# Kernel optimization log

Measured on AMD Instinct MI355X. Metric: run time of the kernel, lower is better.

Reference implementation:

```python
import jax, jax.numpy as jnp
import numpy as np

H1, W1 = 16, 16  # SparseAttBlock stride
EPS = 1e-5       # BatchNorm eps


def _att(x, wx, bx, wy, by, wo, bo, gamma, beta):
    """DotProductAttBlock: 1x1 q/k projections, full softmax attention over
    the H*W tokens of each (small) block, then 1x1 conv + BatchNorm(train) + ReLU."""
    B, C, H, W = x.shape
    xf = x.reshape(B, C, H * W)                                  # [B,C,N]
    theta = jnp.einsum('mc,bcn->bnm', wx, xf) + bx               # [B,N,fmid]
    psi = jnp.einsum('mc,bcn->bmn', wy, xf) + by[:, None]        # [B,fmid,N]
    alpha = jax.nn.softmax(jnp.einsum('bnm,bmk->bnk', theta, psi), axis=2)  # [B,N,N]
    agg = jnp.einsum('bnk,bck->bcn', alpha, xf)                  # [B,C,N]
    out = jnp.einsum('oc,bcn->bon', wo, agg) + bo[:, None]       # [B,fout,N]
    # BatchNorm2d in training mode: biased batch stats over (batch, spatial)
    mean = out.mean(axis=(0, 2), keepdims=True)
    var = ((out - mean) ** 2).mean(axis=(0, 2), keepdims=True)
    out = (out - mean) * jax.lax.rsqrt(var + EPS) * gamma[:, None] + beta[:, None]
    return jax.nn.relu(out).reshape(B, -1, H, W)


def _forward(x, p1, p2):
    B, C, H, W = x.shape
    h2, w2 = H // H1, W // W1
    # pass 1: attention within each (H1,W1) block, blocks folded into batch
    xb = x.reshape(B, C, H1, h2, W1, w2).transpose(0, 3, 5, 1, 2, 4)
    xb = xb.reshape(B * h2 * w2, C, H1, W1)
    xb = _att(xb, *p1)
    # pass 2: attention across the (h2,w2) block grid
    xb = xb.reshape(B, h2, w2, C, H1, W1).transpose(0, 4, 5, 3, 1, 2)
    xb = xb.reshape(B * H1 * W1, C, h2, w2)
    xb = _att(xb, *p2)
    return xb.reshape(B, H1, W1, C, h2, w2).transpose(0, 3, 1, 4, 2, 5).reshape(B, C, H, W)


def setup_inputs() -> dict:
    key = jax.random.key(0)
    ks = jax.random.split(key, 20)
    B, C, FMID, H, W = 4, 128, 64, 256, 256
    s = 0.05
    d = {'x': jax.random.normal(ks[0], (B, C, H, W), jnp.float32)}
    d['w1x'] = jax.random.normal(ks[1], (FMID, C), jnp.float32) * s
    d['b1x'] = jax.random.normal(ks[2], (FMID,), jnp.float32) * s
    d['w1y'] = jax.random.normal(ks[3], (FMID, C), jnp.float32) * s
    d['b1y'] = jax.random.normal(ks[4], (FMID,), jnp.float32) * s
    d['w1o'] = jax.random.normal(ks[5], (C, C), jnp.float32) * s
    d['b1o'] = jax.random.normal(ks[6], (C,), jnp.float32) * s
    d['g1'] = jnp.ones((C,), jnp.float32)
    d['be1'] = jnp.zeros((C,), jnp.float32)
    d['w2x'] = jax.random.normal(ks[7], (FMID, C), jnp.float32) * s
    d['b2x'] = jax.random.normal(ks[8], (FMID,), jnp.float32) * s
    d['w2y'] = jax.random.normal(ks[9], (FMID, C), jnp.float32) * s
    d['b2y'] = jax.random.normal(ks[10], (FMID,), jnp.float32) * s
    d['w2o'] = jax.random.normal(ks[11], (C, C), jnp.float32) * s
    d['b2o'] = jax.random.normal(ks[12], (C,), jnp.float32) * s
    d['g2'] = jnp.ones((C,), jnp.float32)
    d['be2'] = jnp.zeros((C,), jnp.float32)
    return d


def reference(x, w1x, b1x, w1y, b1y, w1o, b1o, g1, be1,
              w2x, b2x, w2y, b2y, w2o, b2o, g2, be2):
    p1 = (w1x, b1x, w1y, b1y, w1o, b1o, g1, be1)
    p2 = (w2x, b2x, w2y, b2y, w2o, b2o, g2, be2)
    return _forward(x, p1, p2)
```

## Files before the change

### kernel.cpp

```cpp
#include <hip/hip_runtime.h>

typedef _Float16 f16;
typedef f16 f16x2 __attribute__((ext_vector_type(2)));
typedef f16 f16x4 __attribute__((ext_vector_type(4)));
typedef f16 f16x8 __attribute__((ext_vector_type(8)));
typedef float f32x4 __attribute__((ext_vector_type(4)));

#define MFMA16(a, b, c) __builtin_amdgcn_mfma_f32_16x16x32_f16((a), (b), (c), 0, 0, 0)

__device__ __forceinline__ f16x4 lo4(f16x8 v) { return __builtin_shufflevector(v, v, 0, 1, 2, 3); }
__device__ __forceinline__ f16x4 hi4(f16x8 v) { return __builtin_shufflevector(v, v, 4, 5, 6, 7); }

#define OFF_YL  65536
#define OFF_SC  98304
#define OFF_SST 139264
#define LDS_ATT 140288

__global__ __launch_bounds__(512) void repack_kernel(const float* __restrict__ x,
                                                     f16* __restrict__ Xall) {
    __shared__ f16 XT[128 * 264];
    const int tid = threadIdx.x, g = blockIdx.x;
    const int b = g >> 8, i1 = (g >> 4) & 15, i2 = g & 15;
    const int h = i1 * 16 + i2;
    {
        const int c = tid >> 2, wq = (tid & 3) * 64;
        const float* src = x + (((size_t)b * 128 + c) * 256 + h) * 256 + wq;
        f16* dst = XT + c * 264 + wq;
#pragma unroll
        for (int i = 0; i < 16; ++i) {
            f32x4 v = *(const f32x4*)(src + i * 4);
            f16x4 o = {(f16)v[0], (f16)v[1], (f16)v[2], (f16)v[3]};
            *(f16x4*)(dst + i * 4) = o;
        }
    }
    __syncthreads();
    {
        const int w = tid >> 1, ch = (tid & 1) * 64;
        const int j1 = w >> 4, j2 = w & 15;
        f16* dst = Xall + (((size_t)b * 256 + i2 * 16 + j2) * 256 + i1 * 16 + j1) * 128 + ch;
#pragma unroll
        for (int i = 0; i < 8; ++i) {
            f16x8 v;
#pragma unroll
            for (int j = 0; j < 8; ++j) v[j] = XT[(ch + i * 8 + j) * 264 + w];
            *(f16x8*)(dst + i * 8) = v;
        }
    }
}

__global__ void wconv_kernel(const float* __restrict__ w1x, const float* __restrict__ w1y,
                             const float* __restrict__ w1o, const float* __restrict__ w2x,
                             const float* __restrict__ w2y, const float* __restrict__ w2o,
                             f16* __restrict__ Wf) {
    int i = blockIdx.x * 256 + threadIdx.x;
    int p = i >> 15, r = (i >> 7) & 255, c = i & 127;
    const float* s;
    if (p == 0) s = (r < 128) ? w1o + r * 128 : (r < 192) ? w1x + (r - 128) * 128
                                                          : w1y + (r - 192) * 128;
    else        s = (r < 128) ? w2o + r * 128 : (r < 192) ? w2x + (r - 128) * 128
                                                          : w2y + (r - 192) * 128;
    Wf[i] = (f16)s[c];
}

template <int PASS>
__global__ __launch_bounds__(512, 2) void att_kernel(
    const f16* __restrict__ Xin, const f16* __restrict__ Wf, const float* __restrict__ bq,
    const float* __restrict__ bk, const float* __restrict__ bo, const float* __restrict__ bnab,
    f16* __restrict__ Uout, float* __restrict__ gstats, int t_stride, int s_stride) {
    __shared__ __align__(16) char smem[LDS_ATT];
    float* SST = (float*)(smem + OFF_SST);
    const int tid = threadIdx.x;
    const int w = tid >> 6, l = tid & 63, lq = l >> 4, lr = l & 15;
    const int g = blockIdx.x, R0 = w * 32;
    char* scb = smem + OFF_SC + w * 5120;
    const unsigned swz = (unsigned)((lr & 7) << 4);

    if (tid < 256) SST[tid] = 0.f;

#pragma unroll
    for (int j = 0; j < 8; ++j) {
        int byte = (j * 512 + tid) * 16;
        f16x8 v = *(const f16x8*)((const char*)Wf + byte);
        *(f16x8*)(smem + (byte ^ (((byte >> 8) & 7) << 4))) = v;
    }

    const f16* src = Xin + (size_t)g * 32768;
    f16x8 afr[2][4];
#pragma unroll
    for (int mt = 0; mt < 2; ++mt)
#pragma unroll
        for (int ks = 0; ks < 4; ++ks)
            afr[mt][ks] = *(const f16x8*)(src + (R0 + mt * 16 + lr) * 128 + ks * 32 + lq * 8);
    if constexpr (PASS == 2) {
#pragma unroll
        for (int ks = 0; ks < 4; ++ks) {
            const int c0 = ks * 32 + lq * 8;
            f32x4 a0 = *(const f32x4*)(bnab + c0), a1 = *(const f32x4*)(bnab + c0 + 4);
            f32x4 s0 = *(const f32x4*)(bnab + 128 + c0), s1 = *(const f32x4*)(bnab + 132 + c0);
#pragma unroll
            for (int mt = 0; mt < 2; ++mt) {
                f16x8 v = afr[mt][ks];
#pragma unroll
                for (int j = 0; j < 4; ++j) {
                    v[j]     = (f16)fmaxf(a0[j] * (float)v[j]     + s0[j], 0.f);
                    v[j + 4] = (f16)fmaxf(a1[j] * (float)v[j + 4] + s1[j], 0.f);
                }
                afr[mt][ks] = v;
            }
        }
    }
    __syncthreads();

    unsigned wb[4];
#pragma unroll
    for (int ks = 0; ks < 4; ++ks) wb[ks] = (unsigned)((lr * 256 + ks * 64 + lq * 16) ^ swz);

    {
        f32x4 aT[2][4] = {}, aP[2][4] = {};
#pragma unroll
        for (int ks = 0; ks < 4; ++ks) {
            f16x8 Bq[4], Bk[4];
#pragma unroll
            for (int nt = 0; nt < 4; ++nt) {
                Bq[nt] = *(const f16x8*)(smem + wb[ks] + (8 + nt) * 4096);
                Bk[nt] = *(const f16x8*)(smem + wb[ks] + (12 + nt) * 4096);
            }
#pragma unroll
            for (int nt = 0; nt < 4; ++nt)
#pragma unroll
                for (int mt = 0; mt < 2; ++mt) {
                    aT[mt][nt] = MFMA16(afr[mt][ks], Bq[nt], aT[mt][nt]);
                    aP[mt][nt] = MFMA16(afr[mt][ks], Bk[nt], aP[mt][nt]);
                }
        }
        float bqv[4], bkv[4];
#pragma unroll
        for (int nt = 0; nt < 4; ++nt) { bqv[nt] = bq[nt * 16 + lr]; bkv[nt] = bk[nt * 16 + lr]; }
#pragma unroll
        for (int mt = 0; mt < 2; ++mt)
#pragma unroll
            for (int nt = 0; nt < 4; ++nt)
#pragma unroll
                for (int r = 0; r < 4; ++r) {
                    int tl = mt * 16 + lq * 4 + r;
                    int m2 = (nt * 16 + lr) * 2;
                    *(f16*)(scb + ((unsigned)(tl * 128 + m2) ^ (unsigned)((tl & 7) << 4))) =
                        (f16)(aT[mt][nt][r] + bqv[nt]);
                    int k = R0 + tl;
                    *(f16*)(smem + OFF_YL + ((unsigned)(k * 128 + m2) ^ (unsigned)((k & 7) << 4))) =
                        (f16)(aP[mt][nt][r] + bkv[nt]);
                }
    }

    f32x4 aV[2][8] = {};
#pragma unroll
    for (int ks = 0; ks < 4; ++ks) {
        f16x8 Bo[8];
#pragma unroll
        for (int ct = 0; ct < 8; ++ct) Bo[ct] = *(const f16x8*)(smem + wb[ks] + ct * 4096);
#pragma unroll
        for (int ct = 0; ct < 8; ++ct)
#pragma unroll
            for (int mt = 0; mt < 2; ++mt) aV[mt][ct] = MFMA16(afr[mt][ks], Bo[ct], aV[mt][ct]);
    }
    __syncthreads();

    {
        float bov[8];
#pragma unroll
        for (int ct = 0; ct < 8; ++ct) bov[ct] = bo[ct * 16 + lr];
#pragma unroll
        for (int ct = 0; ct < 8; ++ct)
#pragma unroll
            for (int mt = 0; mt < 2; ++mt)
#pragma unroll
                for (int r = 0; r < 4; ++r) {
                    int t = R0 + mt * 16 + lq * 4 + r;
                    *(f16*)(smem + ((unsigned)(lr * 512 + ct * 8192 + t * 2) ^ swz)) =
                        (f16)(aV[mt][ct][r] + bov[ct]);
                }
    }
    __syncthreads();

    f16x8 tb[2][2];
#pragma unroll
    for (int tt = 0; tt < 2; ++tt)
#pragma unroll
        for (int ks = 0; ks < 2; ++ks)
            tb[tt][ks] = *(const f16x8*)(scb +
                ((unsigned)(lr * 128 + tt * 2048 + ks * 64 + lq * 16) ^ swz));

    unsigned yb[2], vb[2];
#pragma unroll
    for (int ks = 0; ks < 2; ++ks) yb[ks] = (unsigned)((lr * 128 + ks * 64 + lq * 16) ^ swz);
#pragma unroll
    for (int p = 0; p < 2; ++p) vb[p] = (unsigned)((lr * 512 + p * 64 + lq * 16) ^ swz);

    const size_t ub = (size_t)(g >> 8) * 8388608 + (size_t)(g & 255) * (size_t)s_stride;

#pragma unroll
    for (int tt = 0; tt < 2; ++tt) {
        f32x4 s[16] = {};
#pragma unroll
        for (int kt = 0; kt < 16; ++kt)
#pragma unroll
            for (int ks = 0; ks < 2; ++ks) {
                f16x8 ay = *(const f16x8*)(smem + OFF_YL + yb[ks] + kt * 2048);
                s[kt] = MFMA16(ay, tb[tt][ks], s[kt]);
            }
        float mx = -1e30f;
#pragma unroll
        for (int kt = 0; kt < 16; ++kt)
            mx = fmaxf(mx, fmaxf(fmaxf(s[kt][0], s[kt][1]), fmaxf(s[kt][2], s[kt][3])));
        mx = fmaxf(mx, __shfl_xor(mx, 16));
        mx = fmaxf(mx, __shfl_xor(mx, 32));
        float sum = 0.f;
#pragma unroll
        for (int kt = 0; kt < 16; ++kt)
#pragma unroll
            for (int r = 0; r < 4; ++r) {
                float p = __expf(s[kt][r] - mx);
                s[kt][r] = p;
                sum += p;
            }
        sum += __shfl_xor(sum, 16);
        sum += __shfl_xor(sum, 32);
        const float rs = 1.f / sum;

        f32x4 o[8] = {};
#pragma unroll
        for (int kc = 0; kc < 8; ++kc) {
            char* slot = scb + (kc & 1) * 1280;
#pragma unroll
            for (int h = 0; h < 2; ++h) {
                f32x4 sv = s[kc * 2 + h];
                f16x4 pv = {(f16)(sv[0] * rs), (f16)(sv[1] * rs),
                            (f16)(sv[2] * rs), (f16)(sv[3] * rs)};
                *(f16x4*)(slot + lr * 80 + h * 32 + lq * 8) = pv;
            }
            f16x8 ap = *(const f16x8*)(slot + lr * 80 + lq * 16);
#pragma unroll
            for (int ct = 0; ct < 8; ++ct) {
                f16x8 bv = *(const f16x8*)(smem + vb[kc & 1] + ct * 8192 + (kc >> 1) * 128);
                o[ct] = MFMA16(ap, bv, o[ct]);
            }
        }

#pragma unroll
        for (int ct = 0; ct < 8; ++ct) {
            float ss = (o[ct][0] + o[ct][1]) + (o[ct][2] + o[ct][3]);
            float sq = o[ct][0] * o[ct][0] + o[ct][1] * o[ct][1] +
                       o[ct][2] * o[ct][2] + o[ct][3] * o[ct][3];
            ss += __shfl_xor(ss, 16); ss += __shfl_xor(ss, 32);
            sq += __shfl_xor(sq, 16); sq += __shfl_xor(sq, 32);
            if (lq == 0) {
                atomicAdd(&SST[ct * 16 + lr], ss);
                atomicAdd(&SST[128 + ct * 16 + lr], sq);
            }
        }
#pragma unroll
        for (int ct = 0; ct < 8; ++ct)
#pragma unroll
            for (int r = 0; r < 4; ++r) {
                int tl = lq * 4 + r;
                *(f16*)(scb + ((unsigned)(tl * 256 + (ct * 16 + lr) * 2) ^
                               (unsigned)((tl & 7) << 4))) = (f16)o[ct][r];
            }
#pragma unroll
        for (int i = 0; i < 4; ++i) {
            int tl = i * 4 + lq;
            f16x8 v8 = *(const f16x8*)(scb + ((unsigned)(tl * 256 + lr * 16) ^
                                              (unsigned)((tl & 7) << 4)));
            *(f16x8*)(Uout + ub + (size_t)(R0 + tt * 16 + tl) * (size_t)t_stride + lr * 8) = v8;
        }
    }
    __syncthreads();
    if (tid < 256) atomicAdd(&gstats[tid], SST[tid]);
}

__global__ void bnfix_kernel(const float* __restrict__ gstats, const float* __restrict__ gamma,
                             const float* __restrict__ beta, float* __restrict__ ab) {
    int c = threadIdx.x;
    if (c < 128) {
        const float inv = 1.f / 262144.f;
        float mean = gstats[c] * inv;
        float var = gstats[128 + c] * inv - mean * mean;
        float rstd = rsqrtf(var + 1e-5f);
        float a = gamma[c] * rstd;
        ab[c] = a;
        ab[128 + c] = beta[c] - mean * a;
    }
}

__global__ __launch_bounds__(256) void final_kernel(const f16* __restrict__ U2,
                                                    const float* __restrict__ ab,
                                                    float* __restrict__ out) {
    __shared__ f16 L[256 * 132];
    const int tid = threadIdx.x, g = blockIdx.x;
    const int b = g >> 8, i1 = (g >> 4) & 15, j1 = g & 15;
    const f16* src = U2 + (size_t)g * 32768;
#pragma unroll
    for (int e = 0; e < 16; ++e) {
        int u = e * 2048 + tid * 8;
        int row = u >> 7, c0 = u & 127;
        f16x8 v = *(const f16x8*)(src + u);
        f16* dst = L + row * 132 + c0;
        *(f16x4*)dst = lo4(v);
        *(f16x4*)(dst + 4) = hi4(v);
    }
    __syncthreads();
    const int j2 = tid & 15, bu = tid >> 4;
#pragma unroll 4
    for (int k = 0; k < 128; ++k) {
        int unit = bu + k * 16;
        int c = unit & 127, i2 = unit >> 7;
        float a = ab[c], bb = ab[128 + c];
        float v = fmaxf(a * (float)L[(i2 * 16 + j2) * 132 + c] + bb, 0.f);
        out[(((size_t)b * 128 + c) * 256 + i1 * 16 + i2) * 256 + j1 * 16 + j2] = v;
    }
}

extern "C" void kernel_launch(void* const* d_in, const int* in_sizes, int n_in, void* d_out,
                              int out_size, void* d_ws, size_t ws_size, hipStream_t stream) {
    (void)in_sizes; (void)n_in; (void)out_size; (void)ws_size;
    const float* x = (const float*)d_in[0];
    const float* w1x = (const float*)d_in[1];
    const float* b1x = (const float*)d_in[2];
    const float* w1y = (const float*)d_in[3];
    const float* b1y = (const float*)d_in[4];
    const float* w1o = (const float*)d_in[5];
    const float* b1o = (const float*)d_in[6];
    const float* g1 = (const float*)d_in[7];
    const float* be1 = (const float*)d_in[8];
    const float* w2x = (const float*)d_in[9];
    const float* b2x = (const float*)d_in[10];
    const float* w2y = (const float*)d_in[11];
    const float* b2y = (const float*)d_in[12];
    const float* w2o = (const float*)d_in[13];
    const float* b2o = (const float*)d_in[14];
    const float* g2 = (const float*)d_in[15];
    const float* be2 = (const float*)d_in[16];

    f16* Xall = (f16*)d_out;
    f16* U1 = (f16*)((char*)d_out + 67108864);
    f16* U2 = (f16*)d_ws;
    f16* Wbf = (f16*)((char*)d_ws + 67108864);
    float* gstats = (float*)((char*)d_ws + 67108864 + 131072);
    float* bnab = gstats + 512;

    hipMemsetAsync(gstats, 0, 2048, stream);
    wconv_kernel<<<256, 256, 0, stream>>>(w1x, w1y, w1o, w2x, w2y, w2o, Wbf);
    repack_kernel<<<1024, 512, 0, stream>>>(x, Xall);

    att_kernel<1><<<1024, 512, 0, stream>>>(Xall, Wbf, b1x, b1y, b1o, (const float*)nullptr, U1,
                                            gstats, 32768, 128);
    bnfix_kernel<<<1, 128, 0, stream>>>(gstats, g1, be1, bnab);
    att_kernel<2><<<1024, 512, 0, stream>>>(U1, Wbf + 32768, b2x, b2y, b2o, bnab, U2,
                                            gstats + 256, 128, 32768);
    bnfix_kernel<<<1, 128, 0, stream>>>(gstats + 256, g2, be2, bnab + 256);
    final_kernel<<<1024, 256, 0, stream>>>(U2, bnab + 256, (float*)d_out);
}
```

Baseline: 307.8 us.

## Interleave both row tiles in attention MFMA loops and pack f16 conversions

The attention kernel now computes scores for both 16-row query tiles in one loop, so each loaded key fragment feeds two MFMAs. Likewise, each V fragment loaded in the P·V loop is reused for both tiles. f16 conversions use packed cvt_pkrtz with vector stores, and s_setprio raises wave priority around the MFMA bursts. This cuts LDS reads and conversion instructions, but doubles the live score and accumulator registers, which may raise register pressure or cause spills. Rounding also changes from round-to-nearest to round-toward-zero.

```diff
diff --git a/kernel.cpp b/kernel.cpp
--- a/kernel.cpp
+++ b/kernel.cpp
@@ -10,6 +10,12 @@
 
 __device__ __forceinline__ f16x4 lo4(f16x8 v) { return __builtin_shufflevector(v, v, 0, 1, 2, 3); }
 __device__ __forceinline__ f16x4 hi4(f16x8 v) { return __builtin_shufflevector(v, v, 4, 5, 6, 7); }
+
+__device__ __forceinline__ f16x4 pk4(float a, float b, float c, float d) {
+    f16x2 lo = __builtin_bit_cast(f16x2, __builtin_amdgcn_cvt_pkrtz(a, b));
+    f16x2 hi = __builtin_bit_cast(f16x2, __builtin_amdgcn_cvt_pkrtz(c, d));
+    return f16x4{lo[0], lo[1], hi[0], hi[1]};
+}
 
 #define OFF_YL  65536
 #define OFF_SC  98304
@@ -172,13 +178,12 @@
 #pragma unroll
         for (int ct = 0; ct < 8; ++ct)
 #pragma unroll
-            for (int mt = 0; mt < 2; ++mt)
-#pragma unroll
-                for (int r = 0; r < 4; ++r) {
-                    int t = R0 + mt * 16 + lq * 4 + r;
-                    *(f16*)(smem + ((unsigned)(lr * 512 + ct * 8192 + t * 2) ^ swz)) =
-                        (f16)(aV[mt][ct][r] + bov[ct]);
-                }
+            for (int mt = 0; mt < 2; ++mt) {
+                int t0 = R0 + mt * 16 + lq * 4;
+                f16x4 pv = pk4(aV[mt][ct][0] + bov[ct], aV[mt][ct][1] + bov[ct],
+                               aV[mt][ct][2] + bov[ct], aV[mt][ct][3] + bov[ct]);
+                *(f16x4*)(smem + ((unsigned)(lr * 512 + ct * 8192 + t0 * 2) ^ swz)) = pv;
+            }
     }
     __syncthreads();
 
@@ -196,22 +201,26 @@
 #pragma unroll
     for (int p = 0; p < 2; ++p) vb[p] = (unsigned)((lr * 512 + p * 64 + lq * 16) ^ swz);
 
-    const size_t ub = (size_t)(g >> 8) * 8388608 + (size_t)(g & 255) * (size_t)s_stride;
-
+    f32x4 s[2][16] = {};
+    __builtin_amdgcn_s_setprio(1);
+#pragma unroll
+    for (int kt = 0; kt < 16; ++kt)
+#pragma unroll
+        for (int ks = 0; ks < 2; ++ks) {
+            f16x8 ay = *(const f16x8*)(smem + OFF_YL + yb[ks] + kt * 2048);
+            s[0][kt] = MFMA16(ay, tb[0][ks], s[0][kt]);
+            s[1][kt] = MFMA16(ay, tb[1][ks], s[1][kt]);
+        }
+    __builtin_amdgcn_s_setprio(0);
+
+    f16x4 p16[2][16];
 #pragma unroll
     for (int tt = 0; tt < 2; ++tt) {
-        f32x4 s[16] = {};
+        float mx = -1e30f;
 #pragma unroll
         for (int kt = 0; kt < 16; ++kt)
-#pragma unroll
-            for (int ks = 0; ks < 2; ++ks) {
-                f16x8 ay = *(const f16x8*)(smem + OFF_YL + yb[ks] + kt * 2048);
-                s[kt] = MFMA16(ay, tb[tt][ks], s[kt]);
-            }
-        float mx = -1e30f;
-#pragma unroll
-        for (int kt = 0; kt < 16; ++kt)
-            mx = fmaxf(mx, fmaxf(fmaxf(s[kt][0], s[kt][1]), fmaxf(s[kt][2], s[kt][3])));
+            mx = fmaxf(mx, fmaxf(fmaxf(s[tt][kt][0], s[tt][kt][1]),
+                                 fmaxf(s[tt][kt][2], s[tt][kt][3])));
         mx = fmaxf(mx, __shfl_xor(mx, 16));
         mx = fmaxf(mx, __shfl_xor(mx, 32));
         float sum = 0.f;
@@ -219,38 +228,49 @@
         for (int kt = 0; kt < 16; ++kt)
 #pragma unroll
             for (int r = 0; r < 4; ++r) {
-                float p = __expf(s[kt][r] - mx);
-                s[kt][r] = p;
+                float p = __expf(s[tt][kt][r] - mx);
+                s[tt][kt][r] = p;
                 sum += p;
             }
         sum += __shfl_xor(sum, 16);
         sum += __shfl_xor(sum, 32);
         const float rs = 1.f / sum;
-
-        f32x4 o[8] = {};
-#pragma unroll
-        for (int kc = 0; kc < 8; ++kc) {
-            char* slot = scb + (kc & 1) * 1280;
-#pragma unroll
-            for (int h = 0; h < 2; ++h) {
-                f32x4 sv = s[kc * 2 + h];
-                f16x4 pv = {(f16)(sv[0] * rs), (f16)(sv[1] * rs),
-                            (f16)(sv[2] * rs), (f16)(sv[3] * rs)};
-                *(f16x4*)(slot + lr * 80 + h * 32 + lq * 8) = pv;
-            }
-            f16x8 ap = *(const f16x8*)(slot + lr * 80 + lq * 16);
-#pragma unroll
-            for (int ct = 0; ct < 8; ++ct) {
-                f16x8 bv = *(const f16x8*)(smem + vb[kc & 1] + ct * 8192 + (kc >> 1) * 128);
-                o[ct] = MFMA16(ap, bv, o[ct]);
-            }
-        }
-
+#pragma unroll
+        for (int kt = 0; kt < 16; ++kt)
+            p16[tt][kt] = pk4(s[tt][kt][0] * rs, s[tt][kt][1] * rs,
+                              s[tt][kt][2] * rs, s[tt][kt][3] * rs);
+    }
+
+    f32x4 o[2][8] = {};
+#pragma unroll
+    for (int kc = 0; kc < 8; ++kc) {
+#pragma unroll
+        for (int tt = 0; tt < 2; ++tt) {
+            char* slot = scb + tt * 1280;
+#pragma unroll
+            for (int h = 0; h < 2; ++h)
+                *(f16x4*)(slot + lr * 80 + h * 32 + lq * 8) = p16[tt][kc * 2 + h];
+        }
+        f16x8 ap0 = *(const f16x8*)(scb + lr * 80 + lq * 16);
+        f16x8 ap1 = *(const f16x8*)(scb + 1280 + lr * 80 + lq * 16);
+        __builtin_amdgcn_s_setprio(1);
 #pragma unroll
         for (int ct = 0; ct < 8; ++ct) {
-            float ss = (o[ct][0] + o[ct][1]) + (o[ct][2] + o[ct][3]);
-            float sq = o[ct][0] * o[ct][0] + o[ct][1] * o[ct][1] +
-                       o[ct][2] * o[ct][2] + o[ct][3] * o[ct][3];
+            f16x8 bv = *(const f16x8*)(smem + vb[kc & 1] + ct * 8192 + (kc >> 1) * 128);
+            o[0][ct] = MFMA16(ap0, bv, o[0][ct]);
+            o[1][ct] = MFMA16(ap1, bv, o[1][ct]);
+        }
+        __builtin_amdgcn_s_setprio(0);
+    }
+
+    const size_t ub = (size_t)(g >> 8) * 8388608 + (size_t)(g & 255) * (size_t)s_stride;
+#pragma unroll
+    for (int tt = 0; tt < 2; ++tt) {
+#pragma unroll
+        for (int ct = 0; ct < 8; ++ct) {
+            float ss = (o[tt][ct][0] + o[tt][ct][1]) + (o[tt][ct][2] + o[tt][ct][3]);
+            float sq = o[tt][ct][0] * o[tt][ct][0] + o[tt][ct][1] * o[tt][ct][1] +
+                       o[tt][ct][2] * o[tt][ct][2] + o[tt][ct][3] * o[tt][ct][3];
             ss += __shfl_xor(ss, 16); ss += __shfl_xor(ss, 32);
             sq += __shfl_xor(sq, 16); sq += __shfl_xor(sq, 32);
             if (lq == 0) {
@@ -264,7 +284,7 @@
             for (int r = 0; r < 4; ++r) {
                 int tl = lq * 4 + r;
                 *(f16*)(scb + ((unsigned)(tl * 256 + (ct * 16 + lr) * 2) ^
-                               (unsigned)((tl & 7) << 4))) = (f16)o[ct][r];
+                               (unsigned)((tl & 7) << 4))) = (f16)o[tt][ct][r];
             }
 #pragma unroll
         for (int i = 0; i < 4; ++i) {
@@ -348,7 +368,7 @@
     float* gstats = (float*)((char*)d_ws + 67108864 + 131072);
     float* bnab = gstats + 512;
 
-    hipMemsetAsync(gstats, 0, 2048, stream);
+    (void)hipMemsetAsync(gstats, 0, 2048, stream);
     wconv_kernel<<<256, 256, 0, stream>>>(w1x, w1y, w1o, w2x, w2y, w2o, Wbf);
     repack_kernel<<<1024, 512, 0, stream>>>(x, Xall);
 
```

After: 299.5 us. -2.7%, faster.

## Switch attention kernel to 32x32x16 MFMA with pre-swizzled fragment layouts

Applied to the files above, without the earlier changes.

Rewrites the attention kernel to use 32x32x16 MFMA tiles instead of 16x16x32. Weights are pre-packed by wconv into the per-lane fragment order so they can be read straight from LDS. Softmax probabilities are now fed to the PV MFMA through permlane32_swap in registers instead of a round trip through LDS, and s_setprio hints are added around the MFMA loops. The aim is fewer LDS transactions and shuffles and better MFMA throughput, at the cost of larger accumulator register footprints that may raise pressure at 2 blocks per CU.

```diff
diff --git a/kernel.cpp b/kernel.cpp
--- a/kernel.cpp
+++ b/kernel.cpp
@@ -5,16 +5,27 @@
 typedef f16 f16x4 __attribute__((ext_vector_type(4)));
 typedef f16 f16x8 __attribute__((ext_vector_type(8)));
 typedef float f32x4 __attribute__((ext_vector_type(4)));
-
-#define MFMA16(a, b, c) __builtin_amdgcn_mfma_f32_16x16x32_f16((a), (b), (c), 0, 0, 0)
-
+typedef float f32x16 __attribute__((ext_vector_type(16)));
+typedef unsigned int u32;
+typedef u32 u32x2 __attribute__((ext_vector_type(2)));
+typedef u32 u32x4 __attribute__((ext_vector_type(4)));
+
+#define MFMA32(a, b, c) __builtin_amdgcn_mfma_f32_32x32x16_f16((a), (b), (c), 0, 0, 0)
+
+__device__ __forceinline__ u32 pk2(float a, float b) {
+    return __builtin_bit_cast(u32, __builtin_amdgcn_cvt_pkrtz(a, b));
+}
+__device__ __forceinline__ f16x4 pk4(float a, float b, float c, float d) {
+    u32x2 t = {pk2(a, b), pk2(c, d)};
+    return __builtin_bit_cast(f16x4, t);
+}
 __device__ __forceinline__ f16x4 lo4(f16x8 v) { return __builtin_shufflevector(v, v, 0, 1, 2, 3); }
 __device__ __forceinline__ f16x4 hi4(f16x8 v) { return __builtin_shufflevector(v, v, 4, 5, 6, 7); }
 
-#define OFF_YL  65536
+#define OFF_Y   65536
 #define OFF_SC  98304
-#define OFF_SST 139264
-#define LDS_ATT 140288
+#define OFF_SST 131072
+#define LDS_ATT 132096
 
 __global__ __launch_bounds__(512) void repack_kernel(const float* __restrict__ x,
                                                      f16* __restrict__ Xall) {
@@ -53,12 +64,15 @@
                              const float* __restrict__ w2y, const float* __restrict__ w2o,
                              f16* __restrict__ Wf) {
     int i = blockIdx.x * 256 + threadIdx.x;
-    int p = i >> 15, r = (i >> 7) & 255, c = i & 127;
+    int p = i >> 15, idx = i & 32767;
+    int j = idx & 7, lane = (idx >> 3) & 63, ks = (idx >> 9) & 7, r = idx >> 12;
+    int row = r * 32 + (lane & 31);
+    int c = ks * 16 + (lane >> 5) * 8 + j;
     const float* s;
-    if (p == 0) s = (r < 128) ? w1o + r * 128 : (r < 192) ? w1x + (r - 128) * 128
-                                                          : w1y + (r - 192) * 128;
-    else        s = (r < 128) ? w2o + r * 128 : (r < 192) ? w2x + (r - 128) * 128
-                                                          : w2y + (r - 192) * 128;
+    if (p == 0) s = (row < 128) ? w1o + row * 128 : (row < 192) ? w1x + (row - 128) * 128
+                                                               : w1y + (row - 192) * 128;
+    else        s = (row < 128) ? w2o + row * 128 : (row < 192) ? w2x + (row - 128) * 128
+                                                               : w2y + (row - 192) * 128;
     Wf[i] = (f16)s[c];
 }
 
@@ -70,208 +84,185 @@
     __shared__ __align__(16) char smem[LDS_ATT];
     float* SST = (float*)(smem + OFF_SST);
     const int tid = threadIdx.x;
-    const int w = tid >> 6, l = tid & 63, lq = l >> 4, lr = l & 15;
+    const int w = tid >> 6, l = tid & 63, hl = l >> 5, l31 = l & 31;
     const int g = blockIdx.x, R0 = w * 32;
-    char* scb = smem + OFF_SC + w * 5120;
-    const unsigned swz = (unsigned)((lr & 7) << 4);
+    char* scb = smem + OFF_SC + w * 4096;
 
     if (tid < 256) SST[tid] = 0.f;
 
 #pragma unroll
     for (int j = 0; j < 8; ++j) {
         int byte = (j * 512 + tid) * 16;
-        f16x8 v = *(const f16x8*)((const char*)Wf + byte);
-        *(f16x8*)(smem + (byte ^ (((byte >> 8) & 7) << 4))) = v;
-    }
-
-    const f16* src = Xin + (size_t)g * 32768;
-    f16x8 afr[2][4];
-#pragma unroll
-    for (int mt = 0; mt < 2; ++mt)
-#pragma unroll
-        for (int ks = 0; ks < 4; ++ks)
-            afr[mt][ks] = *(const f16x8*)(src + (R0 + mt * 16 + lr) * 128 + ks * 32 + lq * 8);
+        *(f16x8*)(smem + byte) = *(const f16x8*)((const char*)Wf + byte);
+    }
+
+    const f16* src = Xin + (size_t)g * 32768 + (R0 + l31) * 128 + hl * 8;
+    f16x8 afr[8];
+#pragma unroll
+    for (int ks = 0; ks < 8; ++ks) afr[ks] = *(const f16x8*)(src + ks * 16);
     if constexpr (PASS == 2) {
 #pragma unroll
-        for (int ks = 0; ks < 4; ++ks) {
-            const int c0 = ks * 32 + lq * 8;
+        for (int ks = 0; ks < 8; ++ks) {
+            const int c0 = ks * 16 + hl * 8;
             f32x4 a0 = *(const f32x4*)(bnab + c0), a1 = *(const f32x4*)(bnab + c0 + 4);
             f32x4 s0 = *(const f32x4*)(bnab + 128 + c0), s1 = *(const f32x4*)(bnab + 132 + c0);
-#pragma unroll
-            for (int mt = 0; mt < 2; ++mt) {
-                f16x8 v = afr[mt][ks];
-#pragma unroll
-                for (int j = 0; j < 4; ++j) {
-                    v[j]     = (f16)fmaxf(a0[j] * (float)v[j]     + s0[j], 0.f);
-                    v[j + 4] = (f16)fmaxf(a1[j] * (float)v[j + 4] + s1[j], 0.f);
-                }
-                afr[mt][ks] = v;
+            f16x8 v = afr[ks];
+#pragma unroll
+            for (int j = 0; j < 4; ++j) {
+                v[j]     = (f16)fmaxf(a0[j] * (float)v[j]     + s0[j], 0.f);
+                v[j + 4] = (f16)fmaxf(a1[j] * (float)v[j + 4] + s1[j], 0.f);
             }
-        }
-    }
-    __syncthreads();
-
-    unsigned wb[4];
-#pragma unroll
-    for (int ks = 0; ks < 4; ++ks) wb[ks] = (unsigned)((lr * 256 + ks * 64 + lq * 16) ^ swz);
-
+            afr[ks] = v;
+        }
+    }
+    __syncthreads();
+
+    f32x16 aT[2] = {}, aP[2] = {};
+#pragma unroll
+    for (int ks = 0; ks < 8; ++ks)
+#pragma unroll
+        for (int nt = 0; nt < 2; ++nt) {
+            f16x8 Bq = *(const f16x8*)(smem + (((4 + nt) * 8 + ks) * 64 + l) * 16);
+            f16x8 Bk = *(const f16x8*)(smem + (((6 + nt) * 8 + ks) * 64 + l) * 16);
+            aT[nt] = MFMA32(afr[ks], Bq, aT[nt]);
+            aP[nt] = MFMA32(afr[ks], Bk, aP[nt]);
+        }
     {
-        f32x4 aT[2][4] = {}, aP[2][4] = {};
+        const int lf = (l31 >> 3) & 1;
+        const int msub = l31 >> 4;
+        const int jb = (l31 & 7) * 2;
+#pragma unroll
+        for (int nt = 0; nt < 2; ++nt) {
+            float bqv = bq[nt * 32 + l31], bkv = bk[nt * 32 + l31];
+            char* bT = scb + (((nt * 2 + msub) * 64) + 32 * lf) * 16 + jb;
+            char* bY = smem + OFF_Y + (((w * 4 + nt * 2 + msub) * 64) + 32 * lf) * 16 + jb;
+#pragma unroll
+            for (int r = 0; r < 16; ++r) {
+                int tl = (r & 3) + 8 * (r >> 2) + 4 * hl;
+                *(f16*)(bT + tl * 16) = (f16)(aT[nt][r] + bqv);
+                *(f16*)(bY + tl * 16) = (f16)(aP[nt][r] + bkv);
+            }
+        }
+    }
+    f16x8 tb[4];
+#pragma unroll
+    for (int ks = 0; ks < 4; ++ks) tb[ks] = *(const f16x8*)(scb + (ks * 64 + l) * 16);
+
+    f32x16 aV[4] = {};
+#pragma unroll
+    for (int ks = 0; ks < 8; ++ks)
+#pragma unroll
+        for (int ct = 0; ct < 4; ++ct) {
+            f16x8 Bo = *(const f16x8*)(smem + ((ct * 8 + ks) * 64 + l) * 16);
+            aV[ct] = MFMA32(afr[ks], Bo, aV[ct]);
+        }
+    __syncthreads();
+
+#pragma unroll
+    for (int ct = 0; ct < 4; ++ct) {
+        float bov = bo[ct * 32 + l31];
+#pragma unroll
+        for (int q = 0; q < 4; ++q) {
+            int ts = 2 * w + (q >> 1);
+            f16x4 pv = pk4(aV[ct][4 * q + 0] + bov, aV[ct][4 * q + 1] + bov,
+                           aV[ct][4 * q + 2] + bov, aV[ct][4 * q + 3] + bov);
+            *(f16x4*)(smem + (((ts * 4 + ct) * 64) + l31 + 32 * (q & 1)) * 16 + 8 * hl) = pv;
+        }
+    }
+    __syncthreads();
+
+    f32x16 s[8] = {};
+    __builtin_amdgcn_s_setprio(1);
+#pragma unroll
+    for (int kt = 0; kt < 8; ++kt)
 #pragma unroll
         for (int ks = 0; ks < 4; ++ks) {
-            f16x8 Bq[4], Bk[4];
-#pragma unroll
-            for (int nt = 0; nt < 4; ++nt) {
-                Bq[nt] = *(const f16x8*)(smem + wb[ks] + (8 + nt) * 4096);
-                Bk[nt] = *(const f16x8*)(smem + wb[ks] + (12 + nt) * 4096);
+            f16x8 ay = *(const f16x8*)(smem + OFF_Y + (((kt * 4 + ks) * 64) + l) * 16);
+            s[kt] = MFMA32(ay, tb[ks], s[kt]);
+        }
+    __builtin_amdgcn_s_setprio(0);
+
+    float mx = -1e30f;
+#pragma unroll
+    for (int kt = 0; kt < 8; ++kt) {
+        float m0 = fmaxf(fmaxf(s[kt][0], s[kt][1]), fmaxf(s[kt][2], s[kt][3]));
+        float m1 = fmaxf(fmaxf(s[kt][4], s[kt][5]), fmaxf(s[kt][6], s[kt][7]));
+        float m2 = fmaxf(fmaxf(s[kt][8], s[kt][9]), fmaxf(s[kt][10], s[kt][11]));
+        float m3 = fmaxf(fmaxf(s[kt][12], s[kt][13]), fmaxf(s[kt][14], s[kt][15]));
+        mx = fmaxf(mx, fmaxf(fmaxf(m0, m1), fmaxf(m2, m3)));
+    }
+    mx = fmaxf(mx, __shfl_xor(mx, 32));
+    float sum = 0.f;
+#pragma unroll
+    for (int kt = 0; kt < 8; ++kt)
+#pragma unroll
+        for (int e = 0; e < 16; ++e) {
+            float p = __expf(s[kt][e] - mx);
+            s[kt][e] = p;
+            sum += p;
+        }
+    sum += __shfl_xor(sum, 32);
+    const float rs = 1.f / sum;
+
+    f32x16 o[4] = {};
+#pragma unroll
+    for (int kt = 0; kt < 8; ++kt) {
+#pragma unroll
+        for (int ks = 0; ks < 2; ++ks) {
+            u32 a0 = pk2(s[kt][8 * ks + 0] * rs, s[kt][8 * ks + 1] * rs);
+            u32 a1 = pk2(s[kt][8 * ks + 2] * rs, s[kt][8 * ks + 3] * rs);
+            u32 b0 = pk2(s[kt][8 * ks + 4] * rs, s[kt][8 * ks + 5] * rs);
+            u32 b1 = pk2(s[kt][8 * ks + 6] * rs, s[kt][8 * ks + 7] * rs);
+            u32x2 r0 = __builtin_amdgcn_permlane32_swap(a0, b0, false, false);
+            u32x2 r1 = __builtin_amdgcn_permlane32_swap(a1, b1, false, false);
+            u32x4 aw = {r0.x, r1.x, r0.y, r1.y};
+            f16x8 ap = __builtin_bit_cast(f16x8, aw);
+            __builtin_amdgcn_s_setprio(1);
+#pragma unroll
+            for (int ct = 0; ct < 4; ++ct) {
+                f16x8 bv = *(const f16x8*)(smem + ((((kt * 2 + ks) * 4 + ct) * 64) + l) * 16);
+                o[ct] = MFMA32(ap, bv, o[ct]);
             }
-#pragma unroll
-            for (int nt = 0; nt < 4; ++nt)
-#pragma unroll
-                for (int mt = 0; mt < 2; ++mt) {
-                    aT[mt][nt] = MFMA16(afr[mt][ks], Bq[nt], aT[mt][nt]);
-                    aP[mt][nt] = MFMA16(afr[mt][ks], Bk[nt], aP[mt][nt]);
-                }
-        }
-        float bqv[4], bkv[4];
-#pragma unroll
-        for (int nt = 0; nt < 4; ++nt) { bqv[nt] = bq[nt * 16 + lr]; bkv[nt] = bk[nt * 16 + lr]; }
-#pragma unroll
-        for (int mt = 0; mt < 2; ++mt)
-#pragma unroll
-            for (int nt = 0; nt < 4; ++nt)
-#pragma unroll
-                for (int r = 0; r < 4; ++r) {
-                    int tl = mt * 16 + lq * 4 + r;
-                    int m2 = (nt * 16 + lr) * 2;
-                    *(f16*)(scb + ((unsigned)(tl * 128 + m2) ^ (unsigned)((tl & 7) << 4))) =
-                        (f16)(aT[mt][nt][r] + bqv[nt]);
-                    int k = R0 + tl;
-                    *(f16*)(smem + OFF_YL + ((unsigned)(k * 128 + m2) ^ (unsigned)((k & 7) << 4))) =
-                        (f16)(aP[mt][nt][r] + bkv[nt]);
-                }
-    }
-
-    f32x4 aV[2][8] = {};
-#pragma unroll
-    for (int ks = 0; ks < 4; ++ks) {
-        f16x8 Bo[8];
-#pragma unroll
-        for (int ct = 0; ct < 8; ++ct) Bo[ct] = *(const f16x8*)(smem + wb[ks] + ct * 4096);
-#pragma unroll
-        for (int ct = 0; ct < 8; ++ct)
-#pragma unroll
-            for (int mt = 0; mt < 2; ++mt) aV[mt][ct] = MFMA16(afr[mt][ks], Bo[ct], aV[mt][ct]);
-    }
-    __syncthreads();
-
-    {
-        float bov[8];
-#pragma unroll
-        for (int ct = 0; ct < 8; ++ct) bov[ct] = bo[ct * 16 + lr];
-#pragma unroll
-        for (int ct = 0; ct < 8; ++ct)
-#pragma unroll
-            for (int mt = 0; mt < 2; ++mt)
-#pragma unroll
-                for (int r = 0; r < 4; ++r) {
-                    int t = R0 + mt * 16 + lq * 4 + r;
-                    *(f16*)(smem + ((unsigned)(lr * 512 + ct * 8192 + t * 2) ^ swz)) =
-                        (f16)(aV[mt][ct][r] + bov[ct]);
-                }
-    }
-    __syncthreads();
-
-    f16x8 tb[2][2];
-#pragma unroll
-    for (int tt = 0; tt < 2; ++tt)
-#pragma unroll
-        for (int ks = 0; ks < 2; ++ks)
-            tb[tt][ks] = *(const f16x8*)(scb +
-                ((unsigned)(lr * 128 + tt * 2048 + ks * 64 + lq * 16) ^ swz));
-
-    unsigned yb[2], vb[2];
-#pragma unroll
-    for (int ks = 0; ks < 2; ++ks) yb[ks] = (unsigned)((lr * 128 + ks * 64 + lq * 16) ^ swz);
-#pragma unroll
-    for (int p = 0; p < 2; ++p) vb[p] = (unsigned)((lr * 512 + p * 64 + lq * 16) ^ swz);
+            __builtin_amdgcn_s_setprio(0);
+        }
+    }
+
+#pragma unroll
+    for (int ct = 0; ct < 4; ++ct) {
+        float ss = 0.f, sq = 0.f;
+#pragma unroll
+        for (int e = 0; e < 16; ++e) {
+            float v = o[ct][e];
+            ss += v;
+            sq += v * v;
+        }
+        ss += __shfl_xor(ss, 32);
+        sq += __shfl_xor(sq, 32);
+        if (hl == 0) {
+            atomicAdd(&SST[ct * 32 + l31], ss);
+            atomicAdd(&SST[128 + ct * 32 + l31], sq);
+        }
+    }
 
     const size_t ub = (size_t)(g >> 8) * 8388608 + (size_t)(g & 255) * (size_t)s_stride;
-
-#pragma unroll
-    for (int tt = 0; tt < 2; ++tt) {
-        f32x4 s[16] = {};
-#pragma unroll
-        for (int kt = 0; kt < 16; ++kt)
-#pragma unroll
-            for (int ks = 0; ks < 2; ++ks) {
-                f16x8 ay = *(const f16x8*)(smem + OFF_YL + yb[ks] + kt * 2048);
-                s[kt] = MFMA16(ay, tb[tt][ks], s[kt]);
+#pragma unroll
+    for (int ro = 0; ro < 2; ++ro) {
+#pragma unroll
+        for (int ct = 0; ct < 4; ++ct)
+#pragma unroll
+            for (int rr = 0; rr < 8; ++rr) {
+                int r = ro * 8 + rr;
+                int tl2 = (r & 3) + 8 * ((r >> 2) & 1) + 4 * hl;
+                int c = ct * 32 + l31;
+                *(f16*)(scb + ((tl2 * 256 + c * 2) ^ (((tl2 >> 2) & 3) << 4))) = (f16)o[ct][r];
             }
-        float mx = -1e30f;
-#pragma unroll
-        for (int kt = 0; kt < 16; ++kt)
-            mx = fmaxf(mx, fmaxf(fmaxf(s[kt][0], s[kt][1]), fmaxf(s[kt][2], s[kt][3])));
-        mx = fmaxf(mx, __shfl_xor(mx, 16));
-        mx = fmaxf(mx, __shfl_xor(mx, 32));
-        float sum = 0.f;
-#pragma unroll
-        for (int kt = 0; kt < 16; ++kt)
-#pragma unroll
-            for (int r = 0; r < 4; ++r) {
-                float p = __expf(s[kt][r] - mx);
-                s[kt][r] = p;
-                sum += p;
-            }
-        sum += __shfl_xor(sum, 16);
-        sum += __shfl_xor(sum, 32);
-        const float rs = 1.f / sum;
-
-        f32x4 o[8] = {};
-#pragma unroll
-        for (int kc = 0; kc < 8; ++kc) {
-            char* slot = scb + (kc & 1) * 1280;
-#pragma unroll
-            for (int h = 0; h < 2; ++h) {
-                f32x4 sv = s[kc * 2 + h];
-                f16x4 pv = {(f16)(sv[0] * rs), (f16)(sv[1] * rs),
-                            (f16)(sv[2] * rs), (f16)(sv[3] * rs)};
-                *(f16x4*)(slot + lr * 80 + h * 32 + lq * 8) = pv;
-            }
-            f16x8 ap = *(const f16x8*)(slot + lr * 80 + lq * 16);
-#pragma unroll
-            for (int ct = 0; ct < 8; ++ct) {
-                f16x8 bv = *(const f16x8*)(smem + vb[kc & 1] + ct * 8192 + (kc >> 1) * 128);
-                o[ct] = MFMA16(ap, bv, o[ct]);
-            }
-        }
-
-#pragma unroll
-        for (int ct = 0; ct < 8; ++ct) {
-            float ss = (o[ct][0] + o[ct][1]) + (o[ct][2] + o[ct][3]);
-            float sq = o[ct][0] * o[ct][0] + o[ct][1] * o[ct][1] +
-                       o[ct][2] * o[ct][2] + o[ct][3] * o[ct][3];
-            ss += __shfl_xor(ss, 16); ss += __shfl_xor(ss, 32);
-            sq += __shfl_xor(sq, 16); sq += __shfl_xor(sq, 32);
-            if (lq == 0) {
-                atomicAdd(&SST[ct * 16 + lr], ss);
-                atomicAdd(&SST[128 + ct * 16 + lr], sq);
-            }
-        }
-#pragma unroll
-        for (int ct = 0; ct < 8; ++ct)
-#pragma unroll
-            for (int r = 0; r < 4; ++r) {
-                int tl = lq * 4 + r;
-                *(f16*)(scb + ((unsigned)(tl * 256 + (ct * 16 + lr) * 2) ^
-                               (unsigned)((tl & 7) << 4))) = (f16)o[ct][r];
-            }
 #pragma unroll
         for (int i = 0; i < 4; ++i) {
-            int tl = i * 4 + lq;
-            f16x8 v8 = *(const f16x8*)(scb + ((unsigned)(tl * 256 + lr * 16) ^
-                                              (unsigned)((tl & 7) << 4)));
-            *(f16x8*)(Uout + ub + (size_t)(R0 + tt * 16 + tl) * (size_t)t_stride + lr * 8) = v8;
+            int row = i * 4 + (l >> 4);
+            f16x8 v8 = *(const f16x8*)(scb + ((row * 256 + (l & 15) * 16) ^
+                                              (((row >> 2) & 3) << 4)));
+            int t = R0 + ro * 16 + row;
+            *(f16x8*)(Uout + ub + (size_t)t * (size_t)t_stride + (l & 15) * 8) = v8;
         }
     }
     __syncthreads();
@@ -345,10 +336,10 @@
     f16* U1 = (f16*)((char*)d_out + 67108864);
     f16* U2 = (f16*)d_ws;
     f16* Wbf = (f16*)((char*)d_ws + 67108864);
-    float* gstats = (float*)((char*)d_ws + 67108864 + 131072);
+    float* gstats = (float*)((char*)d_ws + 67108864 + 262144);
     float* bnab = gstats + 512;
 
-    hipMemsetAsync(gstats, 0, 2048, stream);
+    (void)hipMemsetAsync(gstats, 0, 2048, stream);
     wconv_kernel<<<256, 256, 0, stream>>>(w1x, w1y, w1o, w2x, w2y, w2o, Wbf);
     repack_kernel<<<1024, 512, 0, stream>>>(x, Xall);
 
```

After: 269.4 us. -12.5%, faster.
